# Kernel tuning notes

Measured on AMD Instinct MI355X. Metric: run time of the kernel, lower is better.

Reference implementation:

```python
import jax, jax.numpy as jnp
import numpy as np

H = 16
D_MODEL = 1024
D_K = D_MODEL // H


def setup_inputs() -> dict:
    key = jax.random.key(0)
    ks = jax.random.split(key, 11)
    B, S, D = 2, 2048, D_MODEL
    sc = 1.0 / np.sqrt(D)
    return {
        "query": jax.random.normal(ks[0], (B, S, D), jnp.float32),
        "key": jax.random.normal(ks[1], (B, S, D), jnp.float32),
        "value": jax.random.normal(ks[2], (B, S, D), jnp.float32),
        "Wq": jax.random.normal(ks[3], (D, D), jnp.float32) * sc,
        "bq": jnp.zeros((D,), jnp.float32),
        "Wk": jax.random.normal(ks[4], (D, D), jnp.float32) * sc,
        "bk": jnp.zeros((D,), jnp.float32),
        "Wv": jax.random.normal(ks[5], (D, D), jnp.float32) * sc,
        "bv": jnp.zeros((D,), jnp.float32),
        "Wo": jax.random.normal(ks[6], (D, D), jnp.float32) * sc,
        "bo": jnp.zeros((D,), jnp.float32),
    }


def _split_heads(x, B, S):
    # [B,S,D] -> [B,H,S,d_k]
    return x.reshape(B, S, H, D_K).transpose(0, 2, 1, 3)


def reference(query, key, value, Wq, bq, Wk, bk, Wv, bv, Wo, bo):
    B, S, D = query.shape
    q = _split_heads(query @ Wq + bq, B, S)
    k = _split_heads(key @ Wk + bk, B, key.shape[1])
    v = _split_heads(value @ Wv + bv, B, value.shape[1])
    scores = jnp.einsum("bhqd,bhkd->bhqk", q, k) / jnp.sqrt(jnp.asarray(D_K, q.dtype))
    p_attn = jax.nn.softmax(scores, axis=-1)  # dropout is identity at inference
    x = jnp.einsum("bhqk,bhkd->bhqd", p_attn, v)
    x = x.transpose(0, 2, 1, 3).reshape(B, S, H * D_K)
    return x @ Wo + bo
```

## Files before the change

kernel.cpp:

```cpp
#include <hip/hip_runtime.h>

typedef unsigned short u16;
typedef unsigned int   u32;
typedef __bf16 bf16x8 __attribute__((ext_vector_type(8)));
typedef float  f32x4  __attribute__((ext_vector_type(4)));

static constexpr int S_LEN = 2048;
static constexpr int DMODEL = 1024;
static constexpr int NBH = 32;

__device__ __forceinline__ u16 f2bf(float f) {
  u32 u = __float_as_uint(f);
  u += 0x7fffu + ((u >> 16) & 1u);
  return (u16)(u >> 16);
}

__device__ __forceinline__ void gll16(const void* g, void* l) {
  __builtin_amdgcn_global_load_lds(
      (__attribute__((address_space(1))) unsigned int*)(g),
      (__attribute__((address_space(3))) unsigned int*)(l), 16, 0, 0);
}

__device__ __forceinline__ void cvt8(const float* __restrict__ s, u16* __restrict__ d, int o) {
  float4 a = *(const float4*)(s + o);
  float4 b = *(const float4*)(s + o + 4);
  uint4 r;
  r.x = (u32)f2bf(a.x) | ((u32)f2bf(a.y) << 16);
  r.y = (u32)f2bf(a.z) | ((u32)f2bf(a.w) << 16);
  r.z = (u32)f2bf(b.x) | ((u32)f2bf(b.y) << 16);
  r.w = (u32)f2bf(b.z) | ((u32)f2bf(b.w) << 16);
  *(uint4*)(d + o) = r;
}

__global__ __launch_bounds__(256) void convert_in(
    const float* __restrict__ q, const float* __restrict__ k, const float* __restrict__ v,
    u16* __restrict__ qo, u16* __restrict__ ko, u16* __restrict__ vo) {
  int t = blockIdx.x * 256 + threadIdx.x;
  int o = t * 8;
  cvt8(q, qo, o);
  cvt8(k, ko, o);
  cvt8(v, vo, o);
}

__global__ __launch_bounds__(256) void convert_w(
    const float* __restrict__ Wq, const float* __restrict__ Wk,
    const float* __restrict__ Wv, const float* __restrict__ Wo,
    u16* __restrict__ Wqt, u16* __restrict__ Wkt,
    u16* __restrict__ Wvt, u16* __restrict__ Wot) {
  __shared__ __align__(16) u16 t[64][72];
  int z = blockIdx.z;
  const float* W = (z == 0) ? Wq : (z == 1) ? Wk : (z == 2) ? Wv : Wo;
  u16* Wt = (z == 0) ? Wqt : (z == 1) ? Wkt : (z == 2) ? Wvt : Wot;
  int k0 = blockIdx.y * 64, n0 = blockIdx.x * 64;
  int tid = threadIdx.x;
#pragma unroll
  for (int e = 0; e < 4; ++e) {
    int i = e * 256 + tid;
    int r = i >> 4, c4 = (i & 15) * 4;
    float4 vv = *(const float4*)(W + (size_t)(k0 + r) * 1024 + n0 + c4);
    union { u16 u[4]; uint2 w2; } p;
    p.u[0] = f2bf(vv.x); p.u[1] = f2bf(vv.y); p.u[2] = f2bf(vv.z); p.u[3] = f2bf(vv.w);
    *(uint2*)&t[r][c4] = p.w2;
  }
  __syncthreads();
#pragma unroll
  for (int e = 0; e < 2; ++e) {
    int i = e * 256 + tid;
    int rn = i >> 3, c8 = (i & 7) * 8;
    union { u16 u[8]; uint4 w4; } p;
#pragma unroll
    for (int kk = 0; kk < 8; ++kk) p.u[kk] = t[c8 + kk][rn];
    *(uint4*)(Wt + (size_t)(n0 + rn) * 1024 + k0 + c8) = p.w4;
  }
}

__device__ __forceinline__ void gemm_core(
    const u16* __restrict__ A,
    const u16* __restrict__ Bt,
    int K, int m0, int n0,
    u16* As, u16* Bs, f32x4 acc[4][4]) {
  const int tid = threadIdx.x;
  const int l = tid & 63;
  const int g = l >> 4, q16 = l & 15;
  const int wv = tid >> 6;
  const int wr = wv >> 1, wc = wv & 1;
#pragma unroll
  for (int mi = 0; mi < 4; ++mi)
#pragma unroll
    for (int ni = 0; ni < 4; ++ni) acc[mi][ni] = (f32x4){0.f, 0.f, 0.f, 0.f};

  for (int k0 = 0; k0 < K; k0 += 64) {
    __syncthreads();
#pragma unroll
    for (int c = 0; c < 4; ++c) {
      int i = c * 256 + tid;
      int row = i >> 3, ce = (i & 7) * 8;
      gll16(A + (size_t)(m0 + row) * K + k0 + ce, As + i * 8);
      gll16(Bt + (size_t)(n0 + row) * K + k0 + ce, Bs + i * 8);
    }
    __syncthreads();
#pragma unroll
    for (int kb = 0; kb < 2; ++kb) {
      bf16x8 af[4], bf[4];
#pragma unroll
      for (int mi = 0; mi < 4; ++mi)
        af[mi] = *(const bf16x8*)(As + (wr * 64 + mi * 16 + q16) * 64 + kb * 32 + g * 8);
#pragma unroll
      for (int ni = 0; ni < 4; ++ni)
        bf[ni] = *(const bf16x8*)(Bs + (wc * 64 + ni * 16 + q16) * 64 + kb * 32 + g * 8);
#pragma unroll
      for (int mi = 0; mi < 4; ++mi)
#pragma unroll
        for (int ni = 0; ni < 4; ++ni)
          acc[mi][ni] = __builtin_amdgcn_mfma_f32_16x16x32_bf16(af[mi], bf[ni], acc[mi][ni], 0, 0, 0);
    }
  }
}

__global__ __launch_bounds__(256) void gemm_qkv(
    const u16* __restrict__ qA, const u16* __restrict__ kA, const u16* __restrict__ vA,
    const u16* __restrict__ qW, const u16* __restrict__ kW, const u16* __restrict__ vW,
    const float* __restrict__ qb, const float* __restrict__ kb2, const float* __restrict__ vb,
    u16* __restrict__ Qh, u16* __restrict__ Kh, u16* __restrict__ Vh, float qscale) {
  __shared__ __align__(16) u16 As[128 * 64];
  __shared__ __align__(16) u16 Bs[128 * 64];
  int z = blockIdx.z;
  const u16* A   = (z == 0) ? qA : (z == 1) ? kA : vA;
  const u16* Bt  = (z == 0) ? qW : (z == 1) ? kW : vW;
  const float* bias = (z == 0) ? qb : (z == 1) ? kb2 : vb;
  u16* out = (z == 0) ? Qh : (z == 1) ? Kh : Vh;
  float scale = (z == 0) ? qscale : 1.0f;
  int m0 = blockIdx.y * 128, n0 = blockIdx.x * 128;
  f32x4 acc[4][4];
  gemm_core(A, Bt, 1024, m0, n0, As, Bs, acc);

  const int tid = threadIdx.x;
  const int l = tid & 63;
  const int g = l >> 4, q16 = l & 15;
  const int wv = tid >> 6;
  const int wr = wv >> 1, wc = wv & 1;
#pragma unroll
  for (int ni = 0; ni < 4; ++ni) {
    int n = n0 + wc * 64 + ni * 16 + q16;
    float bvv = bias[n];
    int hh = n >> 6, dk = n & 63;
#pragma unroll
    for (int mi = 0; mi < 4; ++mi) {
#pragma unroll
      for (int j = 0; j < 4; ++j) {
        int m = m0 + wr * 64 + mi * 16 + g * 4 + j;
        int b = m >> 11, s = m & 2047;
        float v = (acc[mi][ni][j] + bvv) * scale;
        out[(((size_t)b * 16 + hh) * 2048 + s) * 64 + dk] = f2bf(v);
      }
    }
  }
}

__global__ __launch_bounds__(256) void gemm_out(
    const u16* __restrict__ A, const u16* __restrict__ Bt,
    const float* __restrict__ bias, float* __restrict__ Out) {
  __shared__ __align__(16) u16 As[128 * 64];
  __shared__ __align__(16) u16 Bs[128 * 64];
  int m0 = blockIdx.y * 128, n0 = blockIdx.x * 128;
  f32x4 acc[4][4];
  gemm_core(A, Bt, 1024, m0, n0, As, Bs, acc);

  const int tid = threadIdx.x;
  const int l = tid & 63;
  const int g = l >> 4, q16 = l & 15;
  const int wv = tid >> 6;
  const int wr = wv >> 1, wc = wv & 1;
#pragma unroll
  for (int ni = 0; ni < 4; ++ni) {
    int n = n0 + wc * 64 + ni * 16 + q16;
    float bvv = bias[n];
#pragma unroll
    for (int mi = 0; mi < 4; ++mi) {
#pragma unroll
      for (int j = 0; j < 4; ++j) {
        int m = m0 + wr * 64 + mi * 16 + g * 4 + j;
        Out[(size_t)m * 1024 + n] = acc[mi][ni][j] + bvv;
      }
    }
  }
}

__global__ __launch_bounds__(256) void transpose_v(const u16* __restrict__ Vh, u16* __restrict__ Vt) {
  __shared__ __align__(16) u16 t[64][72];
  int bh = blockIdx.y, s0 = blockIdx.x * 64;
  int tid = threadIdx.x;
#pragma unroll
  for (int e = 0; e < 2; ++e) {
    int i = e * 256 + tid;
    int r = i >> 3, c8 = (i & 7) * 8;
    uint4 vv = *(const uint4*)(Vh + ((size_t)bh * 2048 + s0 + r) * 64 + c8);
    *(uint4*)&t[r][c8] = vv;
  }
  __syncthreads();
#pragma unroll
  for (int e = 0; e < 2; ++e) {
    int i = e * 256 + tid;
    int d = i >> 3, s8 = (i & 7) * 8;
    union { u16 u[8]; uint4 w4; } p;
#pragma unroll
    for (int kk = 0; kk < 8; ++kk) p.u[kk] = t[s8 + kk][d];
    *(uint4*)(Vt + ((size_t)bh * 64 + d) * 2048 + s0 + s8) = p.w4;
  }
}

__global__ __launch_bounds__(256) void attn_kernel(
    const u16* __restrict__ Qh,
    const u16* __restrict__ Kh,
    const u16* __restrict__ Vt,
    u16* __restrict__ Xb) {
  __shared__ __align__(16) u16 Ks[64 * 64];
  __shared__ __align__(16) u16 Vs[64 * 64];
  __shared__ __align__(16) u16 Ps[4][32][72];

  const int tid = threadIdx.x;
  const int l = tid & 63, wv = tid >> 6;
  const int g = l >> 4, q16 = l & 15;
  const int qblk = blockIdx.x, bh = blockIdx.y;
  const int b = bh >> 4, h = bh & 15;
  const int qrow0 = qblk * 128 + wv * 32;

  bf16x8 bq[2][2];
#pragma unroll
  for (int nq = 0; nq < 2; ++nq)
#pragma unroll
    for (int kb = 0; kb < 2; ++kb)
      bq[nq][kb] = *(const bf16x8*)(Qh + ((size_t)bh * 2048 + qrow0 + nq * 16 + q16) * 64 + kb * 32 + g * 8);

  f32x4 x[2][4];
#pragma unroll
  for (int mi = 0; mi < 2; ++mi)
#pragma unroll
    for (int ni = 0; ni < 4; ++ni) x[mi][ni] = (f32x4){0.f, 0.f, 0.f, 0.f};
  float m_run[2] = {-3e38f, -3e38f};
  float l_run[2] = {0.f, 0.f};

  for (int kt = 0; kt < 32; ++kt) {
    const u16* Kg = Kh + ((size_t)bh * 2048 + kt * 64) * 64;
    const u16* Vg = Vt + (size_t)bh * 64 * 2048 + kt * 64;
    __syncthreads();
#pragma unroll
    for (int c = 0; c < 2; ++c) {
      int i = c * 256 + tid;
      int row = i >> 3;
      int lc8 = (i & 7) ^ (row & 7);
      gll16(Kg + row * 64 + lc8 * 8, Ks + i * 8);
      gll16(Vg + row * 2048 + lc8 * 8, Vs + i * 8);
    }
    __syncthreads();

    f32x4 st[4][2];
#pragma unroll
    for (int mi = 0; mi < 4; ++mi)
#pragma unroll
      for (int nq = 0; nq < 2; ++nq) st[mi][nq] = (f32x4){0.f, 0.f, 0.f, 0.f};
#pragma unroll
    for (int mi = 0; mi < 4; ++mi) {
#pragma unroll
      for (int kb = 0; kb < 2; ++kb) {
        int row = mi * 16 + q16;
        int pc8 = (kb * 4 + g) ^ (row & 7);
        bf16x8 ak = *(const bf16x8*)(Ks + row * 64 + pc8 * 8);
#pragma unroll
        for (int nq = 0; nq < 2; ++nq)
          st[mi][nq] = __builtin_amdgcn_mfma_f32_16x16x32_bf16(ak, bq[nq][kb], st[mi][nq], 0, 0, 0);
      }
    }

    float sfq[2];
#pragma unroll
    for (int nq = 0; nq < 2; ++nq) {
      float mx = st[0][nq][0];
#pragma unroll
      for (int mi = 0; mi < 4; ++mi)
#pragma unroll
        for (int j = 0; j < 4; ++j) mx = fmaxf(mx, st[mi][nq][j]);
      mx = fmaxf(mx, __shfl_xor(mx, 16));
      mx = fmaxf(mx, __shfl_xor(mx, 32));
      float mnew = fmaxf(m_run[nq], mx);
      float sf = __builtin_amdgcn_exp2f(m_run[nq] - mnew);
      float rs = 0.f;
#pragma unroll
      for (int mi = 0; mi < 4; ++mi)
#pragma unroll
        for (int j = 0; j < 4; ++j) {
          float p = __builtin_amdgcn_exp2f(st[mi][nq][j] - mnew);
          st[mi][nq][j] = p;
          rs += p;
        }
      rs += __shfl_xor(rs, 16);
      rs += __shfl_xor(rs, 32);
      l_run[nq] = l_run[nq] * sf + rs;
      m_run[nq] = mnew;
      sfq[nq] = sf;
    }

#pragma unroll
    for (int miq = 0; miq < 2; ++miq) {
#pragma unroll
      for (int j = 0; j < 4; ++j) {
        float sfx = __shfl(sfq[miq], g * 4 + j);
#pragma unroll
        for (int ni = 0; ni < 4; ++ni) x[miq][ni][j] *= sfx;
      }
    }

#pragma unroll
    for (int mi = 0; mi < 4; ++mi) {
#pragma unroll
      for (int nq = 0; nq < 2; ++nq) {
        union { u16 u[4]; uint2 w2; } pk;
#pragma unroll
        for (int j = 0; j < 4; ++j) pk.u[j] = f2bf(st[mi][nq][j]);
        *(uint2*)&Ps[wv][nq * 16 + q16][mi * 16 + g * 4] = pk.w2;
      }
    }

#pragma unroll
    for (int kkb = 0; kkb < 2; ++kkb) {
      bf16x8 ap[2];
#pragma unroll
      for (int miq = 0; miq < 2; ++miq)
        ap[miq] = *(const bf16x8*)&Ps[wv][miq * 16 + q16][kkb * 32 + g * 8];
#pragma unroll
      for (int ni = 0; ni < 4; ++ni) {
        int d = ni * 16 + q16;
        int pc8 = (kkb * 4 + g) ^ (d & 7);
        bf16x8 vf = *(const bf16x8*)(Vs + d * 64 + pc8 * 8);
#pragma unroll
        for (int miq = 0; miq < 2; ++miq)
          x[miq][ni] = __builtin_amdgcn_mfma_f32_16x16x32_bf16(ap[miq], vf, x[miq][ni], 0, 0, 0);
      }
    }
  }

  float li[2] = {1.0f / l_run[0], 1.0f / l_run[1]};
#pragma unroll
  for (int miq = 0; miq < 2; ++miq) {
#pragma unroll
    for (int j = 0; j < 4; ++j) {
      float lv = __shfl(li[miq], g * 4 + j);
      int srow = b * 2048 + qblk * 128 + wv * 32 + miq * 16 + g * 4 + j;
#pragma unroll
      for (int ni = 0; ni < 4; ++ni) {
        int col = h * 64 + ni * 16 + q16;
        Xb[(size_t)srow * 1024 + col] = f2bf(x[miq][ni][j] * lv);
      }
    }
  }
}

extern "C" void kernel_launch(void* const* d_in, const int* in_sizes, int n_in,
                              void* d_out, int out_size, void* d_ws, size_t ws_size,
                              hipStream_t stream) {
  (void)in_sizes; (void)n_in; (void)out_size; (void)ws_size;
  const float* q  = (const float*)d_in[0];
  const float* k  = (const float*)d_in[1];
  const float* v  = (const float*)d_in[2];
  const float* Wq = (const float*)d_in[3];
  const float* bq = (const float*)d_in[4];
  const float* Wk = (const float*)d_in[5];
  const float* bk = (const float*)d_in[6];
  const float* Wv = (const float*)d_in[7];
  const float* bv = (const float*)d_in[8];
  const float* Wo = (const float*)d_in[9];
  const float* bo = (const float*)d_in[10];

  char* W = (char*)d_ws;
  const size_t MB = 1ull << 20;
  u16* qbf = (u16*)(W + 0 * MB);
  u16* kbf = (u16*)(W + 8 * MB);
  u16* vbf = (u16*)(W + 16 * MB);
  u16* wqt = (u16*)(W + 24 * MB);
  u16* wkt = (u16*)(W + 26 * MB);
  u16* wvt = (u16*)(W + 28 * MB);
  u16* wot = (u16*)(W + 30 * MB);
  u16* Qh  = (u16*)(W + 32 * MB);
  u16* Kh  = (u16*)(W + 40 * MB);
  u16* Vh  = (u16*)(W + 48 * MB);
  u16* Vtb = (u16*)(W + 56 * MB);
  u16* Xb  = (u16*)(W + 64 * MB);

  convert_in<<<2048, 256, 0, stream>>>(q, k, v, qbf, kbf, vbf);
  convert_w<<<dim3(16, 16, 4), 256, 0, stream>>>(Wq, Wk, Wv, Wo, wqt, wkt, wvt, wot);
  const float QSCALE = 0.125f * 1.4426950408889634f;
  gemm_qkv<<<dim3(8, 32, 3), 256, 0, stream>>>(qbf, kbf, vbf, wqt, wkt, wvt,
                                               bq, bk, bv, Qh, Kh, Vh, QSCALE);
  transpose_v<<<dim3(32, 32), 256, 0, stream>>>(Vh, Vtb);
  attn_kernel<<<dim3(16, 32), 256, 0, stream>>>(Qh, Kh, Vtb, Xb);
  gemm_out<<<dim3(8, 32), 256, 0, stream>>>(Xb, wot, bo, (float*)d_out);
}
```

Before: 177.0 us.

## Double-buffer K/V tiles in attention, use 8 waves, add lazy rescale

The attention kernel now prefetches the next K/V tile into a second LDS buffer while it computes on the current one, with one barrier per iteration instead of two. The block grows to 512 threads, so each wave owns 16 query rows instead of 32. The running-max rescale of the output is skipped unless the new max exceeds the old one by more than 8 (in log2 units). A packed bf16 conversion instruction replaces the manual rounding in the input conversion and the P packing. These changes trade more LDS and smaller per-wave MFMA work for better overlap of loads with compute and less softmax overhead; the lazy rescale relies on exp2 values staying bounded.

```diff
diff --git a/kernel.cpp b/kernel.cpp
--- a/kernel.cpp
+++ b/kernel.cpp
@@ -5,16 +5,18 @@
 typedef __bf16 bf16x8 __attribute__((ext_vector_type(8)));
 typedef float  f32x4  __attribute__((ext_vector_type(4)));
 
-static constexpr int S_LEN = 2048;
-static constexpr int DMODEL = 1024;
-static constexpr int NBH = 32;
-
 __device__ __forceinline__ u16 f2bf(float f) {
   u32 u = __float_as_uint(f);
   u += 0x7fffu + ((u >> 16) & 1u);
   return (u16)(u >> 16);
 }
 
+__device__ __forceinline__ u32 cvt_pk_bf16(float a, float b) {
+  u32 r;
+  asm("v_cvt_pk_bf16_f32 %0, %1, %2" : "=v"(r) : "v"(a), "v"(b));
+  return r;
+}
+
 __device__ __forceinline__ void gll16(const void* g, void* l) {
   __builtin_amdgcn_global_load_lds(
       (__attribute__((address_space(1))) unsigned int*)(g),
@@ -25,10 +27,10 @@
   float4 a = *(const float4*)(s + o);
   float4 b = *(const float4*)(s + o + 4);
   uint4 r;
-  r.x = (u32)f2bf(a.x) | ((u32)f2bf(a.y) << 16);
-  r.y = (u32)f2bf(a.z) | ((u32)f2bf(a.w) << 16);
-  r.z = (u32)f2bf(b.x) | ((u32)f2bf(b.y) << 16);
-  r.w = (u32)f2bf(b.z) | ((u32)f2bf(b.w) << 16);
+  r.x = cvt_pk_bf16(a.x, a.y);
+  r.y = cvt_pk_bf16(a.z, a.w);
+  r.z = cvt_pk_bf16(b.x, b.y);
+  r.w = cvt_pk_bf16(b.z, b.w);
   *(uint4*)(d + o) = r;
 }
 
@@ -101,18 +103,18 @@
     __syncthreads();
 #pragma unroll
     for (int kb = 0; kb < 2; ++kb) {
-      bf16x8 af[4], bf[4];
+      bf16x8 af[4], bfr[4];
 #pragma unroll
       for (int mi = 0; mi < 4; ++mi)
         af[mi] = *(const bf16x8*)(As + (wr * 64 + mi * 16 + q16) * 64 + kb * 32 + g * 8);
 #pragma unroll
       for (int ni = 0; ni < 4; ++ni)
-        bf[ni] = *(const bf16x8*)(Bs + (wc * 64 + ni * 16 + q16) * 64 + kb * 32 + g * 8);
+        bfr[ni] = *(const bf16x8*)(Bs + (wc * 64 + ni * 16 + q16) * 64 + kb * 32 + g * 8);
 #pragma unroll
       for (int mi = 0; mi < 4; ++mi)
 #pragma unroll
         for (int ni = 0; ni < 4; ++ni)
-          acc[mi][ni] = __builtin_amdgcn_mfma_f32_16x16x32_bf16(af[mi], bf[ni], acc[mi][ni], 0, 0, 0);
+          acc[mi][ni] = __builtin_amdgcn_mfma_f32_16x16x32_bf16(af[mi], bfr[ni], acc[mi][ni], 0, 0, 0);
     }
   }
 }
@@ -209,148 +211,132 @@
   }
 }
 
-__global__ __launch_bounds__(256) void attn_kernel(
+__global__ __launch_bounds__(512) void attn_kernel(
     const u16* __restrict__ Qh,
     const u16* __restrict__ Kh,
     const u16* __restrict__ Vt,
     u16* __restrict__ Xb) {
-  __shared__ __align__(16) u16 Ks[64 * 64];
-  __shared__ __align__(16) u16 Vs[64 * 64];
-  __shared__ __align__(16) u16 Ps[4][32][72];
+  __shared__ __align__(16) u16 Ks[2][64 * 64];
+  __shared__ __align__(16) u16 Vs[2][64 * 64];
+  __shared__ __align__(16) u16 Ps[8][16][72];
 
   const int tid = threadIdx.x;
   const int l = tid & 63, wv = tid >> 6;
   const int g = l >> 4, q16 = l & 15;
   const int qblk = blockIdx.x, bh = blockIdx.y;
   const int b = bh >> 4, h = bh & 15;
-  const int qrow0 = qblk * 128 + wv * 32;
-
-  bf16x8 bq[2][2];
-#pragma unroll
-  for (int nq = 0; nq < 2; ++nq)
-#pragma unroll
-    for (int kb = 0; kb < 2; ++kb)
-      bq[nq][kb] = *(const bf16x8*)(Qh + ((size_t)bh * 2048 + qrow0 + nq * 16 + q16) * 64 + kb * 32 + g * 8);
-
-  f32x4 x[2][4];
-#pragma unroll
-  for (int mi = 0; mi < 2; ++mi)
-#pragma unroll
-    for (int ni = 0; ni < 4; ++ni) x[mi][ni] = (f32x4){0.f, 0.f, 0.f, 0.f};
-  float m_run[2] = {-3e38f, -3e38f};
-  float l_run[2] = {0.f, 0.f};
+  const int qrow0 = qblk * 128 + wv * 16;
+
+  const int srow = tid >> 3;
+  const int sc8  = (tid & 7) ^ (srow & 7);
+  const u16* Kbase = Kh + (size_t)bh * 2048 * 64;
+  const u16* Vbase = Vt + (size_t)bh * 64 * 2048;
+
+  bf16x8 bq[2];
+#pragma unroll
+  for (int kb = 0; kb < 2; ++kb)
+    bq[kb] = *(const bf16x8*)(Qh + ((size_t)bh * 2048 + qrow0 + q16) * 64 + kb * 32 + g * 8);
+
+  f32x4 x[4];
+#pragma unroll
+  for (int ni = 0; ni < 4; ++ni) x[ni] = (f32x4){0.f, 0.f, 0.f, 0.f};
+  float m_run = -3e38f, l_run = 0.f;
+
+  gll16(Kbase + (size_t)srow * 64 + sc8 * 8, &Ks[0][tid * 8]);
+  gll16(Vbase + (size_t)srow * 2048 + sc8 * 8, &Vs[0][tid * 8]);
+  asm volatile("s_waitcnt vmcnt(0)" ::: "memory");
+  __builtin_amdgcn_s_barrier();
 
   for (int kt = 0; kt < 32; ++kt) {
-    const u16* Kg = Kh + ((size_t)bh * 2048 + kt * 64) * 64;
-    const u16* Vg = Vt + (size_t)bh * 64 * 2048 + kt * 64;
-    __syncthreads();
-#pragma unroll
-    for (int c = 0; c < 2; ++c) {
-      int i = c * 256 + tid;
-      int row = i >> 3;
-      int lc8 = (i & 7) ^ (row & 7);
-      gll16(Kg + row * 64 + lc8 * 8, Ks + i * 8);
-      gll16(Vg + row * 2048 + lc8 * 8, Vs + i * 8);
-    }
-    __syncthreads();
-
-    f32x4 st[4][2];
+    const int cb = kt & 1, nb = cb ^ 1;
+    if (kt + 1 < 32) {
+      gll16(Kbase + ((size_t)(kt + 1) * 64 + srow) * 64 + sc8 * 8, &Ks[nb][tid * 8]);
+      gll16(Vbase + (size_t)srow * 2048 + (kt + 1) * 64 + sc8 * 8, &Vs[nb][tid * 8]);
+    }
+
+    f32x4 st[4];
+#pragma unroll
+    for (int mi = 0; mi < 4; ++mi) st[mi] = (f32x4){0.f, 0.f, 0.f, 0.f};
+#pragma unroll
+    for (int mi = 0; mi < 4; ++mi) {
+      int row = mi * 16 + q16;
+#pragma unroll
+      for (int kb = 0; kb < 2; ++kb) {
+        int pc8 = (kb * 4 + g) ^ (row & 7);
+        bf16x8 ak = *(const bf16x8*)(&Ks[cb][row * 64 + pc8 * 8]);
+        st[mi] = __builtin_amdgcn_mfma_f32_16x16x32_bf16(ak, bq[kb], st[mi], 0, 0, 0);
+      }
+    }
+
+    float mx = st[0][0];
 #pragma unroll
     for (int mi = 0; mi < 4; ++mi)
 #pragma unroll
-      for (int nq = 0; nq < 2; ++nq) st[mi][nq] = (f32x4){0.f, 0.f, 0.f, 0.f};
+      for (int j = 0; j < 4; ++j) mx = fmaxf(mx, st[mi][j]);
+    mx = fmaxf(mx, __shfl_xor(mx, 16));
+    mx = fmaxf(mx, __shfl_xor(mx, 32));
+
+    float mref, sf;
+    if (__all(mx <= m_run + 8.f)) {
+      mref = m_run; sf = 1.f;
+    } else {
+      mref = fmaxf(m_run, mx);
+      sf = __builtin_amdgcn_exp2f(m_run - mref);
+      m_run = mref;
+#pragma unroll
+      for (int j = 0; j < 4; ++j) {
+        float sfx = __shfl(sf, g * 4 + j);
+#pragma unroll
+        for (int ni = 0; ni < 4; ++ni) x[ni][j] *= sfx;
+      }
+    }
+
+    float rs = 0.f;
+#pragma unroll
+    for (int mi = 0; mi < 4; ++mi)
+#pragma unroll
+      for (int j = 0; j < 4; ++j) {
+        float p = __builtin_amdgcn_exp2f(st[mi][j] - mref);
+        st[mi][j] = p;
+        rs += p;
+      }
+    rs += __shfl_xor(rs, 16);
+    rs += __shfl_xor(rs, 32);
+    l_run = l_run * sf + rs;
+
 #pragma unroll
     for (int mi = 0; mi < 4; ++mi) {
-#pragma unroll
-      for (int kb = 0; kb < 2; ++kb) {
-        int row = mi * 16 + q16;
-        int pc8 = (kb * 4 + g) ^ (row & 7);
-        bf16x8 ak = *(const bf16x8*)(Ks + row * 64 + pc8 * 8);
-#pragma unroll
-        for (int nq = 0; nq < 2; ++nq)
-          st[mi][nq] = __builtin_amdgcn_mfma_f32_16x16x32_bf16(ak, bq[nq][kb], st[mi][nq], 0, 0, 0);
-      }
-    }
-
-    float sfq[2];
-#pragma unroll
-    for (int nq = 0; nq < 2; ++nq) {
-      float mx = st[0][nq][0];
-#pragma unroll
-      for (int mi = 0; mi < 4; ++mi)
-#pragma unroll
-        for (int j = 0; j < 4; ++j) mx = fmaxf(mx, st[mi][nq][j]);
-      mx = fmaxf(mx, __shfl_xor(mx, 16));
-      mx = fmaxf(mx, __shfl_xor(mx, 32));
-      float mnew = fmaxf(m_run[nq], mx);
-      float sf = __builtin_amdgcn_exp2f(m_run[nq] - mnew);
-      float rs = 0.f;
-#pragma unroll
-      for (int mi = 0; mi < 4; ++mi)
-#pragma unroll
-        for (int j = 0; j < 4; ++j) {
-          float p = __builtin_amdgcn_exp2f(st[mi][nq][j] - mnew);
-          st[mi][nq][j] = p;
-          rs += p;
-        }
-      rs += __shfl_xor(rs, 16);
-      rs += __shfl_xor(rs, 32);
-      l_run[nq] = l_run[nq] * sf + rs;
-      m_run[nq] = mnew;
-      sfq[nq] = sf;
-    }
-
-#pragma unroll
-    for (int miq = 0; miq < 2; ++miq) {
-#pragma unroll
-      for (int j = 0; j < 4; ++j) {
-        float sfx = __shfl(sfq[miq], g * 4 + j);
-#pragma unroll
-        for (int ni = 0; ni < 4; ++ni) x[miq][ni][j] *= sfx;
-      }
-    }
-
-#pragma unroll
-    for (int mi = 0; mi < 4; ++mi) {
-#pragma unroll
-      for (int nq = 0; nq < 2; ++nq) {
-        union { u16 u[4]; uint2 w2; } pk;
-#pragma unroll
-        for (int j = 0; j < 4; ++j) pk.u[j] = f2bf(st[mi][nq][j]);
-        *(uint2*)&Ps[wv][nq * 16 + q16][mi * 16 + g * 4] = pk.w2;
-      }
+      uint2 w;
+      w.x = cvt_pk_bf16(st[mi][0], st[mi][1]);
+      w.y = cvt_pk_bf16(st[mi][2], st[mi][3]);
+      *(uint2*)&Ps[wv][q16][mi * 16 + g * 4] = w;
     }
 
 #pragma unroll
     for (int kkb = 0; kkb < 2; ++kkb) {
-      bf16x8 ap[2];
-#pragma unroll
-      for (int miq = 0; miq < 2; ++miq)
-        ap[miq] = *(const bf16x8*)&Ps[wv][miq * 16 + q16][kkb * 32 + g * 8];
+      bf16x8 ap = *(const bf16x8*)&Ps[wv][q16][kkb * 32 + g * 8];
 #pragma unroll
       for (int ni = 0; ni < 4; ++ni) {
         int d = ni * 16 + q16;
         int pc8 = (kkb * 4 + g) ^ (d & 7);
-        bf16x8 vf = *(const bf16x8*)(Vs + d * 64 + pc8 * 8);
-#pragma unroll
-        for (int miq = 0; miq < 2; ++miq)
-          x[miq][ni] = __builtin_amdgcn_mfma_f32_16x16x32_bf16(ap[miq], vf, x[miq][ni], 0, 0, 0);
-      }
-    }
-  }
-
-  float li[2] = {1.0f / l_run[0], 1.0f / l_run[1]};
-#pragma unroll
-  for (int miq = 0; miq < 2; ++miq) {
-#pragma unroll
-    for (int j = 0; j < 4; ++j) {
-      float lv = __shfl(li[miq], g * 4 + j);
-      int srow = b * 2048 + qblk * 128 + wv * 32 + miq * 16 + g * 4 + j;
-#pragma unroll
-      for (int ni = 0; ni < 4; ++ni) {
-        int col = h * 64 + ni * 16 + q16;
-        Xb[(size_t)srow * 1024 + col] = f2bf(x[miq][ni][j] * lv);
-      }
+        bf16x8 vf = *(const bf16x8*)(&Vs[cb][d * 64 + pc8 * 8]);
+        x[ni] = __builtin_amdgcn_mfma_f32_16x16x32_bf16(ap, vf, x[ni], 0, 0, 0);
+      }
+    }
+
+    asm volatile("s_waitcnt vmcnt(0)" ::: "memory");
+    __builtin_amdgcn_s_barrier();
+  }
+
+  float li = 1.0f / l_run;
+#pragma unroll
+  for (int j = 0; j < 4; ++j) {
+    float lv = __shfl(li, g * 4 + j);
+    int srw = b * 2048 + qblk * 128 + wv * 16 + g * 4 + j;
+#pragma unroll
+    for (int ni = 0; ni < 4; ++ni) {
+      int col = h * 64 + ni * 16 + q16;
+      Xb[(size_t)srw * 1024 + col] = f2bf(x[ni][j] * lv);
     }
   }
 }
@@ -392,6 +378,6 @@
   gemm_qkv<<<dim3(8, 32, 3), 256, 0, stream>>>(qbf, kbf, vbf, wqt, wkt, wvt,
                                                bq, bk, bv, Qh, Kh, Vh, QSCALE);
   transpose_v<<<dim3(32, 32), 256, 0, stream>>>(Vh, Vtb);
-  attn_kernel<<<dim3(16, 32), 256, 0, stream>>>(Qh, Kh, Vtb, Xb);
+  attn_kernel<<<dim3(16, 32), 512, 0, stream>>>(Qh, Kh, Vtb, Xb);
   gemm_out<<<dim3(8, 32), 256, 0, stream>>>(Xb, wot, bo, (float*)d_out);
 }
```

New measurement: 154.3 us. -12.8%, faster.
